# Kernel optimization log

Hardware: AMD Instinct MI355X
Metric: run time of the kernel (lower is better)

The kernel has to match this reference:

```python
import jax, jax.numpy as jnp
import numpy as np

B, N, S = 32, 4096, 11          # batch, n_inputs (64x64 feature map), n_slots
D_IN, D, MLP = 512, 512, 2048   # input feat dim, qkv_size, mlp hidden
ITERS = 3                       # num_iterations
EPS_ATTN = 1e-8                 # renormalize epsilon
EPS_LN = 1e-5                   # torch LayerNorm default eps


def layer_norm(x, g, b, eps=EPS_LN):
    mu = jnp.mean(x, axis=-1, keepdims=True)
    var = jnp.mean(jnp.square(x - mu), axis=-1, keepdims=True)
    return (x - mu) * jax.lax.rsqrt(var + eps) * g + b


def setup_inputs() -> dict:
    key = jax.random.key(0)
    ks = jax.random.split(key, 16)
    s = 0.02
    return {
        "slots": jax.random.normal(ks[0], (B, S, D), jnp.float32),
        "inputs": jax.random.normal(ks[1], (B, N, D_IN), jnp.float32),
        # input LayerNorm
        "ln_in_g": jnp.ones((D_IN,), jnp.float32),
        "ln_in_b": jnp.zeros((D_IN,), jnp.float32),
        # k / v projections (with bias, like nn.Linear)
        "Wk": jax.random.normal(ks[2], (D_IN, D), jnp.float32) * s,
        "bk": jnp.zeros((D,), jnp.float32),
        "Wv": jax.random.normal(ks[3], (D_IN, D), jnp.float32) * s,
        "bv": jnp.zeros((D,), jnp.float32),
        # query LayerNorm + bias-free q projection
        "ln_q_g": jnp.ones((D,), jnp.float32),
        "ln_q_b": jnp.zeros((D,), jnp.float32),
        "Wq": jax.random.normal(ks[4], (D, D), jnp.float32) * s,
        # GRUCell: gate order (r, z, n), torch layout [3D, D]
        "W_ih": jax.random.normal(ks[5], (3 * D, D), jnp.float32) * s,
        "b_ih": jnp.zeros((3 * D,), jnp.float32),
        "W_hh": jax.random.normal(ks[6], (3 * D, D), jnp.float32) * s,
        "b_hh": jnp.zeros((3 * D,), jnp.float32),
        # MLP: LN -> Linear -> ReLU -> Linear (no residual in source)
        "ln_m_g": jnp.ones((D,), jnp.float32),
        "ln_m_b": jnp.zeros((D,), jnp.float32),
        "W1": jax.random.normal(ks[7], (D, MLP), jnp.float32) * s,
        "b1": jnp.zeros((MLP,), jnp.float32),
        "W2": jax.random.normal(ks[8], (MLP, D), jnp.float32) * s,
        "b2": jnp.zeros((D,), jnp.float32),
    }


def reference(slots, inputs, ln_in_g, ln_in_b, Wk, bk, Wv, bv,
              ln_q_g, ln_q_b, Wq, W_ih, b_ih, W_hh, b_hh,
              ln_m_g, ln_m_b, W1, b1, W2, b2):
    # inputs LN + k/v projections (computed once, outside the loop)
    x = layer_norm(inputs, ln_in_g, ln_in_b)          # [B, N, D_IN]
    k = x @ Wk + bk                                   # [B, N, D]
    v = x @ Wv + bv                                   # [B, N, D]
    scale = 1.0 / jnp.sqrt(jnp.asarray(D, slots.dtype))

    for _ in range(ITERS):
        # q projection
        q = layer_norm(slots, ln_q_g, ln_q_b) @ Wq    # [B, S, D]
        # inverted attention: softmax over slot (query) axis
        logits = jnp.einsum('bsd,bnd->bsn', q * scale, k)  # [B, S, N]
        attn = jax.nn.softmax(logits, axis=-2)        # over S (inverted)
        # renormalize over keys (mean norm)
        attn = attn / (jnp.sum(attn, axis=-1, keepdims=True) + EPS_ATTN)
        updates = jnp.einsum('bsn,bnd->bsd', attn, v)  # [B, S, D]

        # GRUCell(updates, slots) -- torch semantics, gate order (r, z, n)
        gi = updates @ W_ih.T + b_ih                  # [B, S, 3D]
        gh = slots @ W_hh.T + b_hh                    # [B, S, 3D]
        ir, iz, in_ = jnp.split(gi, 3, axis=-1)
        hr, hz, hn = jnp.split(gh, 3, axis=-1)
        r = jax.nn.sigmoid(ir + hr)
        z = jax.nn.sigmoid(iz + hz)
        n = jnp.tanh(in_ + r * hn)
        slots = (1.0 - z) * n + z * slots

        # MLP (note: source assigns slots = mlp(slots), no residual)
        h = layer_norm(slots, ln_m_g, ln_m_b)
        slots = jax.nn.relu(h @ W1 + b1) @ W2 + b2
    return slots
```

## Files before the change

kernel.cpp:

```cpp
#include <hip/hip_runtime.h>
#include <cstdint>
#include <cstddef>

typedef short bf16x8 __attribute__((ext_vector_type(8)));
typedef float floatx4 __attribute__((ext_vector_type(4)));
typedef unsigned short ushort4v __attribute__((ext_vector_type(4)));

#define LN_EPS 1e-5f
#define ATTN_EPS 1e-8f
#define NCHUNK 16

__device__ __forceinline__ unsigned short f2bf(float f) {
    unsigned int u = __float_as_uint(f);
    u += 0x7fffu + ((u >> 16) & 1u);
    return (unsigned short)(u >> 16);
}

__device__ __forceinline__ void load_lds16(const void* gp, void* lp) {
    __builtin_amdgcn_global_load_lds(
        (__attribute__((address_space(1))) void*)gp,
        (__attribute__((address_space(3))) void*)lp,
        16, 0, 0);
}

template<bool OUT_BF16, bool QDOT>
__global__ __launch_bounds__(256) void ln512_kernel(
        const float* __restrict__ x, const float* __restrict__ g, const float* __restrict__ b,
        void* __restrict__ out, int total_rows, int data_rows, float outscale,
        const float* __restrict__ wqbk, float* __restrict__ cbuf) {
    int row = blockIdx.x * 4 + (threadIdx.x >> 6);
    int lane = threadIdx.x & 63;
    if (row >= total_rows) return;
    int rr = row < data_rows ? row : data_rows - 1;
    const float4* xr = (const float4*)(x + (size_t)rr * 512);
    float4 a0 = xr[lane];
    float4 a1 = xr[lane + 64];
    float s  = a0.x + a0.y + a0.z + a0.w + a1.x + a1.y + a1.z + a1.w;
    float ss = a0.x*a0.x + a0.y*a0.y + a0.z*a0.z + a0.w*a0.w
             + a1.x*a1.x + a1.y*a1.y + a1.z*a1.z + a1.w*a1.w;
    #pragma unroll
    for (int off = 32; off > 0; off >>= 1) {
        s  += __shfl_xor(s, off, 64);
        ss += __shfl_xor(ss, off, 64);
    }
    float mu = s * (1.0f / 512.0f);
    float var = ss * (1.0f / 512.0f) - mu * mu;
    float rstd = rsqrtf(var + LN_EPS);
    float4 g0 = ((const float4*)g)[lane];
    float4 g1 = ((const float4*)g)[lane + 64];
    float4 b0 = ((const float4*)b)[lane];
    float4 b1 = ((const float4*)b)[lane + 64];
    float y[8];
    y[0] = ((a0.x - mu) * rstd * g0.x + b0.x) * outscale;
    y[1] = ((a0.y - mu) * rstd * g0.y + b0.y) * outscale;
    y[2] = ((a0.z - mu) * rstd * g0.z + b0.z) * outscale;
    y[3] = ((a0.w - mu) * rstd * g0.w + b0.w) * outscale;
    y[4] = ((a1.x - mu) * rstd * g1.x + b1.x) * outscale;
    y[5] = ((a1.y - mu) * rstd * g1.y + b1.y) * outscale;
    y[6] = ((a1.z - mu) * rstd * g1.z + b1.z) * outscale;
    y[7] = ((a1.w - mu) * rstd * g1.w + b1.w) * outscale;
    if (QDOT) {
        float4 w0 = ((const float4*)wqbk)[lane];
        float4 w1 = ((const float4*)wqbk)[lane + 64];
        float cd = y[0]*w0.x + y[1]*w0.y + y[2]*w0.z + y[3]*w0.w
                 + y[4]*w1.x + y[5]*w1.y + y[6]*w1.z + y[7]*w1.w;
        #pragma unroll
        for (int off = 32; off > 0; off >>= 1) cd += __shfl_xor(cd, off, 64);
        if (lane == 0) cbuf[row] = cd;
    }
    if (OUT_BF16) {
        unsigned short* orow = (unsigned short*)out + (size_t)row * 512;
        ushort4v o0, o1;
        o0.x = f2bf(y[0]); o0.y = f2bf(y[1]); o0.z = f2bf(y[2]); o0.w = f2bf(y[3]);
        o1.x = f2bf(y[4]); o1.y = f2bf(y[5]); o1.z = f2bf(y[6]); o1.w = f2bf(y[7]);
        *(ushort4v*)(orow + lane * 4) = o0;
        *(ushort4v*)(orow + 256 + lane * 4) = o1;
    } else {
        float* orow = (float*)out + (size_t)row * 512;
        *(float4*)(orow + lane * 4) = make_float4(y[0], y[1], y[2], y[3]);
        *(float4*)(orow + 256 + lane * 4) = make_float4(y[4], y[5], y[6], y[7]);
    }
}

__device__ __forceinline__ void tr32(const float* __restrict__ in, unsigned short* __restrict__ out,
                                     int R, int C, int bx, int by, float (*tile)[33]) {
    int tx = threadIdx.x & 31, ty = threadIdx.x >> 5;
    #pragma unroll
    for (int i = 0; i < 32; i += 8)
        tile[ty + i][tx] = in[(size_t)(by + ty + i) * C + bx + tx];
    __syncthreads();
    #pragma unroll
    for (int i = 0; i < 32; i += 8)
        out[(size_t)(bx + ty + i) * R + by + tx] = f2bf(tile[tx][ty + i]);
}

__device__ __forceinline__ void rowdot512(const float* __restrict__ in, const float* __restrict__ vec,
                                          float* __restrict__ out, int row) {
    int lane = threadIdx.x & 63;
    const float4* r0 = (const float4*)(in + (size_t)row * 512);
    float4 a0 = r0[lane], a1 = r0[lane + 64];
    float4 v0 = ((const float4*)vec)[lane], v1 = ((const float4*)vec)[lane + 64];
    float d = a0.x*v0.x + a0.y*v0.y + a0.z*v0.z + a0.w*v0.w
            + a1.x*v1.x + a1.y*v1.y + a1.z*v1.z + a1.w*v1.w;
    #pragma unroll
    for (int off = 32; off > 0; off >>= 1) d += __shfl_xor(d, off, 64);
    if (lane == 0) out[row] = d;
}

__global__ __launch_bounds__(256) void prep_all(
        const float* __restrict__ Wk, const float* __restrict__ Wq,
        const float* __restrict__ Wv, const float* __restrict__ W_ih,
        const float* __restrict__ W_hh, const float* __restrict__ W1,
        const float* __restrict__ W2, const float* __restrict__ slots_in,
        const float* __restrict__ bk, const float* __restrict__ bv,
        unsigned short* __restrict__ Wk_b, unsigned short* __restrict__ Wq_b,
        unsigned short* __restrict__ Wv_b, unsigned short* __restrict__ Wih_b,
        unsigned short* __restrict__ Whh_b, unsigned short* __restrict__ W1T,
        unsigned short* __restrict__ W2T, unsigned short* __restrict__ slbf,
        float* __restrict__ wqbk, float* __restrict__ bvW) {
    __shared__ float tile[32][33];
    const int b = blockIdx.x;
    const int t = threadIdx.x;
    if (b < 1024) {
        int idx = b * 256 + t; Wk_b[idx] = f2bf(Wk[idx]);
    } else if (b < 2048) {
        int idx = (b - 1024) * 256 + t; Wq_b[idx] = f2bf(Wq[idx]);
    } else if (b < 3072) {
        int idx = (b - 2048) * 256 + t; Wv_b[idx] = f2bf(Wv[idx]);
    } else if (b < 6144) {
        int idx = (b - 3072) * 256 + t; Wih_b[idx] = f2bf(W_ih[idx]);
    } else if (b < 9216) {
        int idx = (b - 6144) * 256 + t; Whh_b[idx] = f2bf(W_hh[idx]);
    } else if (b < 10240) {
        int i = b - 9216;
        tr32(W1, W1T, 512, 2048, (i & 63) * 32, (i >> 6) * 32, tile);
    } else if (b < 11264) {
        int i = b - 10240;
        tr32(W2, W2T, 2048, 512, (i & 15) * 32, (i >> 4) * 32, tile);
    } else if (b < 12032) {
        int idx = (b - 11264) * 256 + t;
        int row = idx >> 9, d = idx & 511;
        int rr = row < 352 ? row : 351;
        slbf[idx] = f2bf(slots_in[(size_t)rr * 512 + d]);
    } else if (b < 12160) {
        int row = (b - 12032) * 4 + (t >> 6);
        rowdot512(Wq, bk, wqbk, row);
    } else {
        int row = (b - 12160) * 4 + (t >> 6);
        rowdot512(W_ih, bv, bvW, row);
    }
}

template<int BMODE, bool RELU, int OUT_MODE>
__device__ __forceinline__ void hgemm_core(
        const unsigned short* __restrict__ A, const unsigned short* __restrict__ Bt,
        const float* __restrict__ bias, const float* __restrict__ bvW,
        const float* __restrict__ coef, float* __restrict__ Cf,
        unsigned short* __restrict__ Cb, int m0, int n0, int N, int K,
        unsigned short* As, unsigned short* Bs) {
    const int t = threadIdx.x;
    const int lane = t & 63;
    const int w = t >> 6;
    const int wm = w >> 1, wn = w & 1;
    const int quad = lane >> 4;
    const int l15 = lane & 15;
    floatx4 acc[2][2];
    #pragma unroll
    for (int i = 0; i < 2; ++i)
        #pragma unroll
        for (int j = 0; j < 2; ++j)
            #pragma unroll
            for (int r = 0; r < 4; ++r) acc[i][j][r] = 0.0f;

    for (int k0 = 0; k0 < K; k0 += 64) {
        #pragma unroll
        for (int p = 0; p < 2; ++p) {
            const int s = p * 256 + t;
            const int row = s >> 3;
            const int c = (s & 7) ^ (row & 7);
            const int ldsoff = (s - lane) * 16;
            load_lds16(A  + (size_t)(m0 + row) * K + k0 + c * 8, (char*)As + ldsoff);
            load_lds16(Bt + (size_t)(n0 + row) * K + k0 + c * 8, (char*)Bs + ldsoff);
        }
        __builtin_amdgcn_s_waitcnt(0);
        __syncthreads();
        #pragma unroll
        for (int h = 0; h < 2; ++h) {
            bf16x8 af[2], bfr[2];
            #pragma unroll
            for (int i = 0; i < 2; ++i) {
                const int row = wm * 32 + i * 16 + l15;
                const int cp = ((h << 2) | quad) ^ (l15 & 7);
                af[i] = *(const bf16x8*)(As + row * 64 + cp * 8);
            }
            #pragma unroll
            for (int j = 0; j < 2; ++j) {
                const int row = wn * 32 + j * 16 + l15;
                const int cp = ((h << 2) | quad) ^ (l15 & 7);
                bfr[j] = *(const bf16x8*)(Bs + row * 64 + cp * 8);
            }
            #pragma unroll
            for (int i = 0; i < 2; ++i)
                #pragma unroll
                for (int j = 0; j < 2; ++j)
                    acc[i][j] = __builtin_amdgcn_mfma_f32_16x16x32_bf16(af[i], bfr[j], acc[i][j], 0, 0, 0);
        }
        __syncthreads();
    }
    #pragma unroll
    for (int j = 0; j < 2; ++j) {
        const int n = n0 + wn * 32 + j * 16 + l15;
        const float bb = (BMODE >= 1) ? bias[n] : 0.0f;
        const float bw = (BMODE == 2) ? bvW[n] : 0.0f;
        #pragma unroll
        for (int i = 0; i < 2; ++i) {
            #pragma unroll
            for (int r = 0; r < 4; ++r) {
                const int m = m0 + wm * 32 + i * 16 + quad * 4 + r;
                float v = acc[i][j][r] + bb;
                if (BMODE == 2) v += coef[m] * bw;
                if (RELU) v = fmaxf(v, 0.0f);
                if (OUT_MODE == 0 || OUT_MODE == 2) Cf[(size_t)m * N + n] = v;
                if (OUT_MODE == 1 || OUT_MODE == 2) Cb[(size_t)m * N + n] = f2bf(v);
            }
        }
    }
}

template<int BMODE, bool RELU, int OUT_MODE>
__global__ __launch_bounds__(256) void hgemm(
        const unsigned short* __restrict__ A, const unsigned short* __restrict__ Bt,
        const float* __restrict__ bias, float* __restrict__ Cf,
        unsigned short* __restrict__ Cb, int N, int K) {
    __shared__ unsigned short As[64 * 64];
    __shared__ unsigned short Bs[64 * 64];
    hgemm_core<BMODE, RELU, OUT_MODE>(A, Bt, bias, nullptr, nullptr, Cf, Cb,
                                      blockIdx.y * 64, blockIdx.x * 64, N, K, As, Bs);
}

__global__ __launch_bounds__(256) void prep_gemms(
        const unsigned short* __restrict__ Wk_b, const unsigned short* __restrict__ Wq_b,
        const unsigned short* __restrict__ Wih_b, const unsigned short* __restrict__ Wv_b,
        unsigned short* __restrict__ WqkT, unsigned short* __restrict__ Wc) {
    __shared__ unsigned short As[64 * 64];
    __shared__ unsigned short Bs[64 * 64];
    if (blockIdx.z == 0) {
        if (blockIdx.y >= 8) return;
        hgemm_core<0, false, 1>(Wk_b, Wq_b, nullptr, nullptr, nullptr, nullptr, WqkT,
                                blockIdx.y * 64, blockIdx.x * 64, 512, 512, As, Bs);
    } else {
        hgemm_core<0, false, 1>(Wih_b, Wv_b, nullptr, nullptr, nullptr, nullptr, Wc,
                                blockIdx.y * 64, blockIdx.x * 64, 512, 512, As, Bs);
    }
}

__global__ __launch_bounds__(256) void gru_gemm(
        const unsigned short* __restrict__ Pn, const unsigned short* __restrict__ slbf,
        const unsigned short* __restrict__ Wc, const unsigned short* __restrict__ Whh,
        const float* __restrict__ bih, const float* __restrict__ bhh,
        const float* __restrict__ bvW, const float* __restrict__ coef,
        float* __restrict__ gi, float* __restrict__ gh) {
    __shared__ unsigned short As[64 * 64];
    __shared__ unsigned short Bs[64 * 64];
    if (blockIdx.z == 0)
        hgemm_core<2, false, 0>(Pn, Wc, bih, bvW, coef, gi, nullptr,
                                blockIdx.y * 64, blockIdx.x * 64, 1536, 512, As, Bs);
    else
        hgemm_core<1, false, 0>(slbf, Whh, bhh, nullptr, nullptr, gh, nullptr,
                                blockIdx.y * 64, blockIdx.x * 64, 1536, 512, As, Bs);
}

__global__ __launch_bounds__(256, 2) void attn_kernel(
        const unsigned short* __restrict__ qp_b, const unsigned short* __restrict__ xln,
        const float* __restrict__ cbuf,
        float* __restrict__ Up, float* __restrict__ rsp) {
    const int b = blockIdx.y;
    const int chunk = blockIdx.x;
    const int w = threadIdx.x >> 6, lane = threadIdx.x & 63;
    const int l15 = lane & 15, quad = lane >> 4;
    const int d0 = lane * 8;
    const int NPC = 4096 / NCHUNK;

    __shared__ float attnlds[4][16][20];
    __shared__ float Us[11 * 512];
    __shared__ float rss[11];

    const unsigned short* qrow = qp_b + (size_t)(b * 11 + (l15 < 11 ? l15 : 10)) * 512 + quad * 8;
    bf16x8 aq[16];
    #pragma unroll
    for (int ks = 0; ks < 16; ++ks) aq[ks] = *(const bf16x8*)(qrow + ks * 32);

    float cb[4];
    #pragma unroll
    for (int r = 0; r < 4; ++r) {
        int s = quad * 4 + r;
        cb[r] = (s < 11) ? cbuf[b * 11 + s] : 0.0f;
    }

    float U[11][8];
    float rs[11];
    #pragma unroll
    for (int s = 0; s < 11; ++s) {
        rs[s] = 0.f;
        #pragma unroll
        for (int j = 0; j < 8; ++j) U[s][j] = 0.f;
    }

    const unsigned short* xbase = xln + ((size_t)b * 4096 + (size_t)chunk * NPC) * 512;

    for (int t = 0; t < NPC / 64; ++t) {
        const int n0 = t * 64 + w * 16;
        const unsigned short* krow = xbase + (size_t)(n0 + l15) * 512 + quad * 8;
        floatx4 c;
        c[0] = c[1] = c[2] = c[3] = 0.0f;
        #pragma unroll
        for (int ks = 0; ks < 16; ++ks) {
            bf16x8 bf = *(const bf16x8*)(krow + ks * 32);
            c = __builtin_amdgcn_mfma_f32_16x16x32_bf16(aq[ks], bf, c, 0, 0, 0);
        }
        float l0 = c[0] + cb[0], l1 = c[1] + cb[1], l2 = c[2] + cb[2], l3 = c[3] + cb[3];
        if (quad == 2) l3 = -1e30f;
        if (quad == 3) { l0 = -1e30f; l1 = -1e30f; l2 = -1e30f; l3 = -1e30f; }
        float mx = fmaxf(fmaxf(l0, l1), fmaxf(l2, l3));
        mx = fmaxf(mx, __shfl_xor(mx, 16, 64));
        mx = fmaxf(mx, __shfl_xor(mx, 32, 64));
        float e0 = __expf(l0 - mx), e1 = __expf(l1 - mx),
              e2 = __expf(l2 - mx), e3 = __expf(l3 - mx);
        float se = e0 + e1 + e2 + e3;
        se += __shfl_xor(se, 16, 64);
        se += __shfl_xor(se, 32, 64);
        float inv = 1.0f / se;
        float4 av = make_float4(e0 * inv, e1 * inv, e2 * inv, e3 * inv);
        *(float4*)&attnlds[w][l15][quad * 4] = av;
        __builtin_amdgcn_wave_barrier();
        for (int nl = 0; nl < 16; ++nl) {
            uint4 kr = *(const uint4*)(xbase + (size_t)(n0 + nl) * 512 + d0);
            float kf[8];
            kf[0] = __uint_as_float(kr.x << 16); kf[1] = __uint_as_float(kr.x & 0xffff0000u);
            kf[2] = __uint_as_float(kr.y << 16); kf[3] = __uint_as_float(kr.y & 0xffff0000u);
            kf[4] = __uint_as_float(kr.z << 16); kf[5] = __uint_as_float(kr.z & 0xffff0000u);
            kf[6] = __uint_as_float(kr.w << 16); kf[7] = __uint_as_float(kr.w & 0xffff0000u);
            float4 a0 = *(const float4*)&attnlds[w][nl][0];
            float4 a1 = *(const float4*)&attnlds[w][nl][4];
            float4 a2 = *(const float4*)&attnlds[w][nl][8];
            float as[11] = {a0.x, a0.y, a0.z, a0.w, a1.x, a1.y, a1.z, a1.w,
                            a2.x, a2.y, a2.z};
            #pragma unroll
            for (int s = 0; s < 11; ++s) {
                rs[s] += as[s];
                #pragma unroll
                for (int j = 0; j < 8; ++j) U[s][j] = fmaf(as[s], kf[j], U[s][j]);
            }
        }
    }

    for (int ph = 0; ph < 4; ++ph) {
        if (w == ph) {
            #pragma unroll
            for (int s = 0; s < 11; ++s) {
                #pragma unroll
                for (int j = 0; j < 8; ++j) {
                    if (ph == 0) Us[s * 512 + d0 + j] = U[s][j];
                    else         Us[s * 512 + d0 + j] += U[s][j];
                }
            }
            if (lane == 0) {
                #pragma unroll
                for (int s = 0; s < 11; ++s) {
                    if (ph == 0) rss[s] = rs[s]; else rss[s] += rs[s];
                }
            }
        }
        __syncthreads();
    }
    float* up = Up + ((size_t)b * NCHUNK + chunk) * 11 * 512;
    for (int idx = threadIdx.x; idx < 11 * 512; idx += 256) up[idx] = Us[idx];
    if (threadIdx.x < 11) rsp[((size_t)b * NCHUNK + chunk) * 11 + threadIdx.x] = rss[threadIdx.x];
}

__global__ __launch_bounds__(256) void attn_reduce(
        const float* __restrict__ Up, const float* __restrict__ rsp,
        unsigned short* __restrict__ Pn, float* __restrict__ coef) {
    const int bs = blockIdx.x;
    if (bs >= 352) {
        for (int d = threadIdx.x; d < 512; d += 256) Pn[(size_t)bs * 512 + d] = 0;
        if (threadIdx.x == 0) coef[bs] = 0.0f;
        return;
    }
    const int b = bs / 11, s = bs - b * 11;
    float rsum = 0.0f;
    #pragma unroll
    for (int c = 0; c < NCHUNK; ++c) rsum += rsp[((size_t)b * NCHUNK + c) * 11 + s];
    const float inv = 1.0f / (rsum + ATTN_EPS);
    if (threadIdx.x == 0) coef[bs] = rsum * inv;
    for (int d = threadIdx.x; d < 512; d += 256) {
        float acc = 0.f;
        #pragma unroll
        for (int c = 0; c < NCHUNK; ++c) acc += Up[(((size_t)b * NCHUNK + c) * 11 + s) * 512 + d];
        Pn[(size_t)bs * 512 + d] = f2bf(acc * inv);
    }
}

__global__ __launch_bounds__(256) void gru_ln(
        const float* __restrict__ gi, const float* __restrict__ gh,
        const float* __restrict__ slots, const float* __restrict__ g,
        const float* __restrict__ b, unsigned short* __restrict__ mln) {
    int row = blockIdx.x * 4 + (threadIdx.x >> 6);
    int lane = threadIdx.x & 63;
    unsigned short* orow = mln + (size_t)row * 512;
    if (row >= 352) {
        ushort4v z; z.x = z.y = z.z = z.w = 0;
        *(ushort4v*)(orow + lane * 4) = z;
        *(ushort4v*)(orow + 256 + lane * 4) = z;
        return;
    }
    const float4* gir = (const float4*)(gi + (size_t)row * 1536);
    const float4* ghr = (const float4*)(gh + (size_t)row * 1536);
    const float4* sr  = (const float4*)(slots + (size_t)row * 512);
    float v[8];
    #pragma unroll
    for (int half = 0; half < 2; ++half) {
        int o = half * 64 + lane;
        float4 ir = gir[o], iz = gir[128 + o], in_ = gir[256 + o];
        float4 hr = ghr[o], hz = ghr[128 + o], hn = ghr[256 + o];
        float4 sv = sr[o];
        float rr[4], zz[4], nn[4];
        rr[0] = 1.f / (1.f + __expf(-(ir.x + hr.x)));
        rr[1] = 1.f / (1.f + __expf(-(ir.y + hr.y)));
        rr[2] = 1.f / (1.f + __expf(-(ir.z + hr.z)));
        rr[3] = 1.f / (1.f + __expf(-(ir.w + hr.w)));
        zz[0] = 1.f / (1.f + __expf(-(iz.x + hz.x)));
        zz[1] = 1.f / (1.f + __expf(-(iz.y + hz.y)));
        zz[2] = 1.f / (1.f + __expf(-(iz.z + hz.z)));
        zz[3] = 1.f / (1.f + __expf(-(iz.w + hz.w)));
        nn[0] = tanhf(in_.x + rr[0] * hn.x);
        nn[1] = tanhf(in_.y + rr[1] * hn.y);
        nn[2] = tanhf(in_.z + rr[2] * hn.z);
        nn[3] = tanhf(in_.w + rr[3] * hn.w);
        v[half * 4 + 0] = (1.f - zz[0]) * nn[0] + zz[0] * sv.x;
        v[half * 4 + 1] = (1.f - zz[1]) * nn[1] + zz[1] * sv.y;
        v[half * 4 + 2] = (1.f - zz[2]) * nn[2] + zz[2] * sv.z;
        v[half * 4 + 3] = (1.f - zz[3]) * nn[3] + zz[3] * sv.w;
    }
    float s = 0.f, ss = 0.f;
    #pragma unroll
    for (int j = 0; j < 8; ++j) { s += v[j]; ss += v[j] * v[j]; }
    #pragma unroll
    for (int off = 32; off > 0; off >>= 1) {
        s  += __shfl_xor(s, off, 64);
        ss += __shfl_xor(ss, off, 64);
    }
    float mu = s * (1.0f / 512.0f);
    float var = ss * (1.0f / 512.0f) - mu * mu;
    float rstd = rsqrtf(var + LN_EPS);
    float4 g0 = ((const float4*)g)[lane], g1 = ((const float4*)g)[lane + 64];
    float4 b0 = ((const float4*)b)[lane], b1 = ((const float4*)b)[lane + 64];
    ushort4v o0, o1;
    o0.x = f2bf((v[0] - mu) * rstd * g0.x + b0.x);
    o0.y = f2bf((v[1] - mu) * rstd * g0.y + b0.y);
    o0.z = f2bf((v[2] - mu) * rstd * g0.z + b0.z);
    o0.w = f2bf((v[3] - mu) * rstd * g0.w + b0.w);
    o1.x = f2bf((v[4] - mu) * rstd * g1.x + b1.x);
    o1.y = f2bf((v[5] - mu) * rstd * g1.y + b1.y);
    o1.z = f2bf((v[6] - mu) * rstd * g1.z + b1.z);
    o1.w = f2bf((v[7] - mu) * rstd * g1.w + b1.w);
    *(ushort4v*)(orow + lane * 4) = o0;
    *(ushort4v*)(orow + 256 + lane * 4) = o1;
}

extern "C" void kernel_launch(void* const* d_in, const int* in_sizes, int n_in,
                              void* d_out, int out_size, void* d_ws, size_t ws_size,
                              hipStream_t stream) {
    const float* slots_in = (const float*)d_in[0];
    const float* inputs   = (const float*)d_in[1];
    const float* ln_in_g  = (const float*)d_in[2];
    const float* ln_in_b  = (const float*)d_in[3];
    const float* Wk  = (const float*)d_in[4];
    const float* bk  = (const float*)d_in[5];
    const float* Wv  = (const float*)d_in[6];
    const float* bv  = (const float*)d_in[7];
    const float* ln_q_g = (const float*)d_in[8];
    const float* ln_q_b = (const float*)d_in[9];
    const float* Wq  = (const float*)d_in[10];
    const float* W_ih = (const float*)d_in[11];
    const float* b_ih = (const float*)d_in[12];
    const float* W_hh = (const float*)d_in[13];
    const float* b_hh = (const float*)d_in[14];
    const float* ln_m_g = (const float*)d_in[15];
    const float* ln_m_b = (const float*)d_in[16];
    const float* W1 = (const float*)d_in[17];
    const float* b1 = (const float*)d_in[18];
    const float* W2 = (const float*)d_in[19];
    const float* b2 = (const float*)d_in[20];

    char* p = (char*)d_ws;
    auto alloc = [&](size_t bytes) { char* r = p; p += (bytes + 255) & ~(size_t)255; return r; };
    unsigned short* xln   = (unsigned short*)alloc(131072ull * 512 * 2);
    unsigned short* Wk_b  = (unsigned short*)alloc(512ull * 512 * 2);
    unsigned short* Wq_b  = (unsigned short*)alloc(512ull * 512 * 2);
    unsigned short* Wv_b  = (unsigned short*)alloc(512ull * 512 * 2);
    unsigned short* Wih_b = (unsigned short*)alloc(1536ull * 512 * 2);
    unsigned short* Whh_b = (unsigned short*)alloc(1536ull * 512 * 2);
    unsigned short* WqkT  = (unsigned short*)alloc(512ull * 512 * 2);
    unsigned short* Wc    = (unsigned short*)alloc(1536ull * 512 * 2);
    unsigned short* W1T   = (unsigned short*)alloc(2048ull * 512 * 2);
    unsigned short* W2T   = (unsigned short*)alloc(512ull * 2048 * 2);
    unsigned short* slq   = (unsigned short*)alloc(384ull * 512 * 2);
    unsigned short* mln   = (unsigned short*)alloc(384ull * 512 * 2);
    unsigned short* Pn    = (unsigned short*)alloc(384ull * 512 * 2);
    unsigned short* slbf  = (unsigned short*)alloc(384ull * 512 * 2);
    unsigned short* h1    = (unsigned short*)alloc(384ull * 2048 * 2);
    unsigned short* qp_b  = (unsigned short*)alloc(384ull * 512 * 2);
    float* slots = (float*)alloc(384ull * 512 * 4);
    float* gi    = (float*)alloc(384ull * 1536 * 4);
    float* gh    = (float*)alloc(384ull * 1536 * 4);
    float* Up    = (float*)alloc((size_t)32 * NCHUNK * 11 * 512 * 4);
    float* rsp   = (float*)alloc((size_t)32 * NCHUNK * 11 * 4);
    float* wqbk  = (float*)alloc(512 * 4);
    float* bvW   = (float*)alloc(1536 * 4);
    float* cbuf  = (float*)alloc(384 * 4);
    float* coef  = (float*)alloc(384 * 4);

    ln512_kernel<true, false><<<dim3(32768), 256, 0, stream>>>(
        inputs, ln_in_g, ln_in_b, xln, 131072, 131072, 1.0f, nullptr, nullptr);
    prep_all<<<dim3(12544), 256, 0, stream>>>(
        Wk, Wq, Wv, W_ih, W_hh, W1, W2, slots_in, bk, bv,
        Wk_b, Wq_b, Wv_b, Wih_b, Whh_b, W1T, W2T, slbf, wqbk, bvW);
    prep_gemms<<<dim3(8, 24, 2), 256, 0, stream>>>(Wk_b, Wq_b, Wih_b, Wv_b, WqkT, Wc);
    hipMemcpyAsync(slots, slots_in, 352ull * 512 * 4, hipMemcpyDeviceToDevice, stream);

    const float qscale = 0.044194173824159216f;
    for (int it = 0; it < 3; ++it) {
        ln512_kernel<true, true><<<dim3(96), 256, 0, stream>>>(
            slots, ln_q_g, ln_q_b, slq, 384, 352, qscale, wqbk, cbuf);
        hgemm<0, false, 1><<<dim3(8, 6), 256, 0, stream>>>(slq, WqkT, nullptr, nullptr, qp_b, 512, 512);
        attn_kernel<<<dim3(NCHUNK, 32), 256, 0, stream>>>(qp_b, xln, cbuf, Up, rsp);
        attn_reduce<<<dim3(384), 256, 0, stream>>>(Up, rsp, Pn, coef);
        gru_gemm<<<dim3(24, 6, 2), 256, 0, stream>>>(Pn, slbf, Wc, Whh_b, b_ih, b_hh, bvW, coef, gi, gh);
        gru_ln<<<dim3(96), 256, 0, stream>>>(gi, gh, slots, ln_m_g, ln_m_b, mln);
        hgemm<1, true, 1><<<dim3(32, 6), 256, 0, stream>>>(mln, W1T, b1, nullptr, h1, 2048, 512);
        hgemm<1, false, 2><<<dim3(8, 6), 256, 0, stream>>>(h1, W2T, b2, slots, slbf, 512, 2048);
    }
    hipMemcpyAsync(d_out, slots, (size_t)out_size * 4, hipMemcpyDeviceToDevice, stream);
}
```

Before: 745.2 us.

## Fuse input LayerNorm into first attention pass and double-buffer GEMM LDS

The standalone input LayerNorm launch is removed. Each first-iteration attention block now normalizes its own chunk of input rows and writes the bf16 result that later iterations reuse. This saves a launch and gives the LN write better cache locality with the attention pass that reads it. Separately, the shared GEMM core now double-buffers its LDS tiles with a partial vmcnt wait, so global-to-LDS loads of the next K-tile overlap MFMA work, at the cost of twice the LDS per block. The slots device copy is also folded into the prep kernel as extra blocks, replacing a memcpy call.

```diff
diff --git a/kernel.cpp b/kernel.cpp
--- a/kernel.cpp
+++ b/kernel.cpp
@@ -117,7 +117,7 @@
         unsigned short* __restrict__ Wv_b, unsigned short* __restrict__ Wih_b,
         unsigned short* __restrict__ Whh_b, unsigned short* __restrict__ W1T,
         unsigned short* __restrict__ W2T, unsigned short* __restrict__ slbf,
-        float* __restrict__ wqbk, float* __restrict__ bvW) {
+        float* __restrict__ wqbk, float* __restrict__ bvW, float* __restrict__ slots) {
     __shared__ float tile[32][33];
     const int b = blockIdx.x;
     const int t = threadIdx.x;
@@ -145,9 +145,12 @@
     } else if (b < 12160) {
         int row = (b - 12032) * 4 + (t >> 6);
         rowdot512(Wq, bk, wqbk, row);
-    } else {
+    } else if (b < 12288) {
         int row = (b - 12160) * 4 + (t >> 6);
         rowdot512(W_ih, bv, bvW, row);
+    } else {
+        int idx = (b - 12288) * 256 + t;
+        slots[idx] = slots_in[idx];
     }
 }
 
@@ -157,7 +160,8 @@
         const float* __restrict__ bias, const float* __restrict__ bvW,
         const float* __restrict__ coef, float* __restrict__ Cf,
         unsigned short* __restrict__ Cb, int m0, int n0, int N, int K,
-        unsigned short* As, unsigned short* Bs) {
+        unsigned short* As0, unsigned short* Bs0,
+        unsigned short* As1, unsigned short* Bs1) {
     const int t = threadIdx.x;
     const int lane = t & 63;
     const int w = t >> 6;
@@ -172,18 +176,18 @@
             #pragma unroll
             for (int r = 0; r < 4; ++r) acc[i][j][r] = 0.0f;
 
-    for (int k0 = 0; k0 < K; k0 += 64) {
+    auto stage = [&](unsigned short* Asd, unsigned short* Bsd, int k0) {
         #pragma unroll
         for (int p = 0; p < 2; ++p) {
             const int s = p * 256 + t;
             const int row = s >> 3;
             const int c = (s & 7) ^ (row & 7);
             const int ldsoff = (s - lane) * 16;
-            load_lds16(A  + (size_t)(m0 + row) * K + k0 + c * 8, (char*)As + ldsoff);
-            load_lds16(Bt + (size_t)(n0 + row) * K + k0 + c * 8, (char*)Bs + ldsoff);
-        }
-        __builtin_amdgcn_s_waitcnt(0);
-        __syncthreads();
+            load_lds16(A  + (size_t)(m0 + row) * K + k0 + c * 8, (char*)Asd + ldsoff);
+            load_lds16(Bt + (size_t)(n0 + row) * K + k0 + c * 8, (char*)Bsd + ldsoff);
+        }
+    };
+    auto compute = [&](const unsigned short* Asr, const unsigned short* Bsr) {
         #pragma unroll
         for (int h = 0; h < 2; ++h) {
             bf16x8 af[2], bfr[2];
@@ -191,13 +195,13 @@
             for (int i = 0; i < 2; ++i) {
                 const int row = wm * 32 + i * 16 + l15;
                 const int cp = ((h << 2) | quad) ^ (l15 & 7);
-                af[i] = *(const bf16x8*)(As + row * 64 + cp * 8);
+                af[i] = *(const bf16x8*)(Asr + row * 64 + cp * 8);
             }
             #pragma unroll
             for (int j = 0; j < 2; ++j) {
                 const int row = wn * 32 + j * 16 + l15;
                 const int cp = ((h << 2) | quad) ^ (l15 & 7);
-                bfr[j] = *(const bf16x8*)(Bs + row * 64 + cp * 8);
+                bfr[j] = *(const bf16x8*)(Bsr + row * 64 + cp * 8);
             }
             #pragma unroll
             for (int i = 0; i < 2; ++i)
@@ -205,8 +209,27 @@
                 for (int j = 0; j < 2; ++j)
                     acc[i][j] = __builtin_amdgcn_mfma_f32_16x16x32_bf16(af[i], bfr[j], acc[i][j], 0, 0, 0);
         }
-        __syncthreads();
-    }
+    };
+
+    const int nk = K >> 6;
+    stage(As0, Bs0, 0);
+    for (int ki = 0; ki < nk; ++ki) {
+        const bool odd = (ki & 1) != 0;
+        unsigned short* Ac = odd ? As1 : As0;
+        unsigned short* Bc = odd ? Bs1 : Bs0;
+        if (ki + 1 < nk) {
+            stage(odd ? As0 : As1, odd ? Bs0 : Bs1, (ki + 1) * 64);
+            asm volatile("s_waitcnt vmcnt(4)" ::: "memory");
+        } else {
+            asm volatile("s_waitcnt vmcnt(0)" ::: "memory");
+        }
+        __builtin_amdgcn_s_barrier();
+        __builtin_amdgcn_sched_barrier(0);
+        compute(Ac, Bc);
+        __builtin_amdgcn_sched_barrier(0);
+        __builtin_amdgcn_s_barrier();
+    }
+
     #pragma unroll
     for (int j = 0; j < 2; ++j) {
         const int n = n0 + wn * 32 + j * 16 + l15;
@@ -232,25 +255,32 @@
         const unsigned short* __restrict__ A, const unsigned short* __restrict__ Bt,
         const float* __restrict__ bias, float* __restrict__ Cf,
         unsigned short* __restrict__ Cb, int N, int K) {
-    __shared__ unsigned short As[64 * 64];
-    __shared__ unsigned short Bs[64 * 64];
+    __shared__ unsigned short As0[64 * 64];
+    __shared__ unsigned short Bs0[64 * 64];
+    __shared__ unsigned short As1[64 * 64];
+    __shared__ unsigned short Bs1[64 * 64];
     hgemm_core<BMODE, RELU, OUT_MODE>(A, Bt, bias, nullptr, nullptr, Cf, Cb,
-                                      blockIdx.y * 64, blockIdx.x * 64, N, K, As, Bs);
+                                      blockIdx.y * 64, blockIdx.x * 64, N, K,
+                                      As0, Bs0, As1, Bs1);
 }
 
 __global__ __launch_bounds__(256) void prep_gemms(
         const unsigned short* __restrict__ Wk_b, const unsigned short* __restrict__ Wq_b,
         const unsigned short* __restrict__ Wih_b, const unsigned short* __restrict__ Wv_b,
         unsigned short* __restrict__ WqkT, unsigned short* __restrict__ Wc) {
-    __shared__ unsigned short As[64 * 64];
-    __shared__ unsigned short Bs[64 * 64];
+    __shared__ unsigned short As0[64 * 64];
+    __shared__ unsigned short Bs0[64 * 64];
+    __shared__ unsigned short As1[64 * 64];
+    __shared__ unsigned short Bs1[64 * 64];
     if (blockIdx.z == 0) {
         if (blockIdx.y >= 8) return;
         hgemm_core<0, false, 1>(Wk_b, Wq_b, nullptr, nullptr, nullptr, nullptr, WqkT,
-                                blockIdx.y * 64, blockIdx.x * 64, 512, 512, As, Bs);
+                                blockIdx.y * 64, blockIdx.x * 64, 512, 512,
+                                As0, Bs0, As1, Bs1);
     } else {
         hgemm_core<0, false, 1>(Wih_b, Wv_b, nullptr, nullptr, nullptr, nullptr, Wc,
-                                blockIdx.y * 64, blockIdx.x * 64, 512, 512, As, Bs);
+                                blockIdx.y * 64, blockIdx.x * 64, 512, 512,
+                                As0, Bs0, As1, Bs1);
     }
 }
 
@@ -260,20 +290,27 @@
         const float* __restrict__ bih, const float* __restrict__ bhh,
         const float* __restrict__ bvW, const float* __restrict__ coef,
         float* __restrict__ gi, float* __restrict__ gh) {
-    __shared__ unsigned short As[64 * 64];
-    __shared__ unsigned short Bs[64 * 64];
+    __shared__ unsigned short As0[64 * 64];
+    __shared__ unsigned short Bs0[64 * 64];
+    __shared__ unsigned short As1[64 * 64];
+    __shared__ unsigned short Bs1[64 * 64];
     if (blockIdx.z == 0)
         hgemm_core<2, false, 0>(Pn, Wc, bih, bvW, coef, gi, nullptr,
-                                blockIdx.y * 64, blockIdx.x * 64, 1536, 512, As, Bs);
+                                blockIdx.y * 64, blockIdx.x * 64, 1536, 512,
+                                As0, Bs0, As1, Bs1);
     else
         hgemm_core<1, false, 0>(slbf, Whh, bhh, nullptr, nullptr, gh, nullptr,
-                                blockIdx.y * 64, blockIdx.x * 64, 1536, 512, As, Bs);
-}
-
+                                blockIdx.y * 64, blockIdx.x * 64, 1536, 512,
+                                As0, Bs0, As1, Bs1);
+}
+
+template<bool LN1>
 __global__ __launch_bounds__(256, 2) void attn_kernel(
-        const unsigned short* __restrict__ qp_b, const unsigned short* __restrict__ xln,
+        const unsigned short* __restrict__ qp_b, unsigned short* xln,
         const float* __restrict__ cbuf,
-        float* __restrict__ Up, float* __restrict__ rsp) {
+        float* __restrict__ Up, float* __restrict__ rsp,
+        const float* __restrict__ inputs,
+        const float* __restrict__ ln_in_g, const float* __restrict__ ln_in_b) {
     const int b = blockIdx.y;
     const int chunk = blockIdx.x;
     const int w = threadIdx.x >> 6, lane = threadIdx.x & 63;
@@ -281,9 +318,47 @@
     const int d0 = lane * 8;
     const int NPC = 4096 / NCHUNK;
 
-    __shared__ float attnlds[4][16][20];
     __shared__ float Us[11 * 512];
+    __shared__ float attnlds[64 * 20];
     __shared__ float rss[11];
+
+    const size_t rowbase = (size_t)b * 4096 + (size_t)chunk * NPC;
+
+    if (LN1) {
+        float4 g0 = ((const float4*)ln_in_g)[lane];
+        float4 g1 = ((const float4*)ln_in_g)[lane + 64];
+        float4 b0 = ((const float4*)ln_in_b)[lane];
+        float4 b1 = ((const float4*)ln_in_b)[lane + 64];
+        for (int r = w; r < NPC; r += 4) {
+            const float4* xr = (const float4*)(inputs + (rowbase + r) * 512);
+            float4 a0 = xr[lane];
+            float4 a1 = xr[lane + 64];
+            float s  = a0.x + a0.y + a0.z + a0.w + a1.x + a1.y + a1.z + a1.w;
+            float ss = a0.x*a0.x + a0.y*a0.y + a0.z*a0.z + a0.w*a0.w
+                     + a1.x*a1.x + a1.y*a1.y + a1.z*a1.z + a1.w*a1.w;
+            #pragma unroll
+            for (int off = 32; off > 0; off >>= 1) {
+                s  += __shfl_xor(s, off, 64);
+                ss += __shfl_xor(ss, off, 64);
+            }
+            float mu = s * (1.0f / 512.0f);
+            float var = ss * (1.0f / 512.0f) - mu * mu;
+            float rstd = rsqrtf(var + LN_EPS);
+            unsigned short* orow = xln + (rowbase + r) * 512;
+            ushort4v o0, o1;
+            o0.x = f2bf((a0.x - mu) * rstd * g0.x + b0.x);
+            o0.y = f2bf((a0.y - mu) * rstd * g0.y + b0.y);
+            o0.z = f2bf((a0.z - mu) * rstd * g0.z + b0.z);
+            o0.w = f2bf((a0.w - mu) * rstd * g0.w + b0.w);
+            o1.x = f2bf((a1.x - mu) * rstd * g1.x + b1.x);
+            o1.y = f2bf((a1.y - mu) * rstd * g1.y + b1.y);
+            o1.z = f2bf((a1.z - mu) * rstd * g1.z + b1.z);
+            o1.w = f2bf((a1.w - mu) * rstd * g1.w + b1.w);
+            *(ushort4v*)(orow + lane * 4) = o0;
+            *(ushort4v*)(orow + 256 + lane * 4) = o1;
+        }
+        __syncthreads();
+    }
 
     const unsigned short* qrow = qp_b + (size_t)(b * 11 + (l15 < 11 ? l15 : 10)) * 512 + quad * 8;
     bf16x8 aq[16];
@@ -306,7 +381,7 @@
         for (int j = 0; j < 8; ++j) U[s][j] = 0.f;
     }
 
-    const unsigned short* xbase = xln + ((size_t)b * 4096 + (size_t)chunk * NPC) * 512;
+    const unsigned short* xbase = xln + rowbase * 512;
 
     for (int t = 0; t < NPC / 64; ++t) {
         const int n0 = t * 64 + w * 16;
@@ -331,7 +406,7 @@
         se += __shfl_xor(se, 32, 64);
         float inv = 1.0f / se;
         float4 av = make_float4(e0 * inv, e1 * inv, e2 * inv, e3 * inv);
-        *(float4*)&attnlds[w][l15][quad * 4] = av;
+        *(float4*)&attnlds[(w * 16 + l15) * 20 + quad * 4] = av;
         __builtin_amdgcn_wave_barrier();
         for (int nl = 0; nl < 16; ++nl) {
             uint4 kr = *(const uint4*)(xbase + (size_t)(n0 + nl) * 512 + d0);
@@ -340,9 +415,10 @@
             kf[2] = __uint_as_float(kr.y << 16); kf[3] = __uint_as_float(kr.y & 0xffff0000u);
             kf[4] = __uint_as_float(kr.z << 16); kf[5] = __uint_as_float(kr.z & 0xffff0000u);
             kf[6] = __uint_as_float(kr.w << 16); kf[7] = __uint_as_float(kr.w & 0xffff0000u);
-            float4 a0 = *(const float4*)&attnlds[w][nl][0];
-            float4 a1 = *(const float4*)&attnlds[w][nl][4];
-            float4 a2 = *(const float4*)&attnlds[w][nl][8];
+            const float* arow = &attnlds[(w * 16 + nl) * 20];
+            float4 a0 = *(const float4*)(arow);
+            float4 a1 = *(const float4*)(arow + 4);
+            float4 a2 = *(const float4*)(arow + 8);
             float as[11] = {a0.x, a0.y, a0.z, a0.w, a1.x, a1.y, a1.z, a1.w,
                             a2.x, a2.y, a2.z};
             #pragma unroll
@@ -521,20 +597,22 @@
     float* cbuf  = (float*)alloc(384 * 4);
     float* coef  = (float*)alloc(384 * 4);
 
-    ln512_kernel<true, false><<<dim3(32768), 256, 0, stream>>>(
-        inputs, ln_in_g, ln_in_b, xln, 131072, 131072, 1.0f, nullptr, nullptr);
-    prep_all<<<dim3(12544), 256, 0, stream>>>(
+    prep_all<<<dim3(12992), 256, 0, stream>>>(
         Wk, Wq, Wv, W_ih, W_hh, W1, W2, slots_in, bk, bv,
-        Wk_b, Wq_b, Wv_b, Wih_b, Whh_b, W1T, W2T, slbf, wqbk, bvW);
+        Wk_b, Wq_b, Wv_b, Wih_b, Whh_b, W1T, W2T, slbf, wqbk, bvW, slots);
     prep_gemms<<<dim3(8, 24, 2), 256, 0, stream>>>(Wk_b, Wq_b, Wih_b, Wv_b, WqkT, Wc);
-    hipMemcpyAsync(slots, slots_in, 352ull * 512 * 4, hipMemcpyDeviceToDevice, stream);
 
     const float qscale = 0.044194173824159216f;
     for (int it = 0; it < 3; ++it) {
         ln512_kernel<true, true><<<dim3(96), 256, 0, stream>>>(
             slots, ln_q_g, ln_q_b, slq, 384, 352, qscale, wqbk, cbuf);
         hgemm<0, false, 1><<<dim3(8, 6), 256, 0, stream>>>(slq, WqkT, nullptr, nullptr, qp_b, 512, 512);
-        attn_kernel<<<dim3(NCHUNK, 32), 256, 0, stream>>>(qp_b, xln, cbuf, Up, rsp);
+        if (it == 0)
+            attn_kernel<true><<<dim3(NCHUNK, 32), 256, 0, stream>>>(
+                qp_b, xln, cbuf, Up, rsp, inputs, ln_in_g, ln_in_b);
+        else
+            attn_kernel<false><<<dim3(NCHUNK, 32), 256, 0, stream>>>(
+                qp_b, xln, cbuf, Up, rsp, nullptr, nullptr, nullptr);
         attn_reduce<<<dim3(384), 256, 0, stream>>>(Up, rsp, Pn, coef);
         gru_gemm<<<dim3(24, 6, 2), 256, 0, stream>>>(Pn, slbf, Wc, Whh_b, b_ih, b_hh, bvW, coef, gi, gh);
         gru_ln<<<dim3(96), 256, 0, stream>>>(gi, gh, slots, ln_m_g, ln_m_b, mln);
```

After: 749.6 us. Within noise of the previous version (+0.6%).
